# Kernel optimization log

Measured on AMD Instinct MI355X. Metric: run time of the kernel, lower is better.

Reference implementation:

```python
import jax, jax.numpy as jnp
import numpy as np

BS, NADJ, N, D_EMB, VOCAB = 2, 2, 2048, 64, 10000
H, F1 = 8, 64
NFEAT = 3 * D_EMB  # 192 = emb0(64) + emb1(64) + local(64)


def setup_inputs() -> dict:
    key = jax.random.key(0)
    ks = jax.random.split(key, 14)
    adj = jax.random.randint(ks[0], (BS, NADJ, N, N), 0, 2).astype(jnp.float32)
    adj = jnp.maximum(adj, jnp.eye(N, dtype=jnp.float32))  # self-loops: no empty softmax rows
    vertices = jax.random.randint(ks[1], (BS, N), 0, VOCAB)
    local_emb = jax.random.normal(ks[2], (BS, N, D_EMB), dtype=jnp.float32)
    xav = lambda fin, fout: (2.0 / (fin + fout)) ** 0.5
    emb0 = jax.random.normal(ks[3], (VOCAB, D_EMB), dtype=jnp.float32) * 0.02
    emb1 = jax.random.normal(ks[4], (VOCAB, D_EMB), dtype=jnp.float32) * 0.02
    w_l0 = jax.random.normal(ks[5], (NADJ, H, NFEAT, F1), dtype=jnp.float32) * xav(NFEAT, F1)
    a_src_l0 = jax.random.normal(ks[6], (NADJ, H, F1, 1), dtype=jnp.float32) * xav(F1, 1)
    a_dst_l0 = jax.random.normal(ks[7], (NADJ, H, F1, 1), dtype=jnp.float32) * xav(F1, 1)
    w_l1 = jax.random.normal(ks[8], (NADJ, H, H * F1, F1), dtype=jnp.float32) * xav(H * F1, F1)
    a_src_l1 = jax.random.normal(ks[9], (NADJ, H, F1, 1), dtype=jnp.float32) * xav(F1, 1)
    a_dst_l1 = jax.random.normal(ks[10], (NADJ, H, F1, 1), dtype=jnp.float32) * xav(F1, 1)
    aw1 = jax.random.normal(ks[11], (NFEAT, F1), dtype=jnp.float32) * xav(NFEAT, F1)
    aw2 = jax.random.normal(ks[12], (F1, F1), dtype=jnp.float32) * xav(F1, F1)
    am = jax.random.normal(ks[13], (F1, 1), dtype=jnp.float32) * xav(F1, 1)
    return dict(hedge_graphs=adj, vertices=vertices, local_emb=local_emb,
                emb0=emb0, emb1=emb1,
                w_l0=w_l0, a_src_l0=a_src_l0, a_dst_l0=a_dst_l0,
                w_l1=w_l1, a_src_l1=a_src_l1, a_dst_l1=a_dst_l1,
                aw1=aw1, aw2=aw2, am=am)


def _gat(h, adj, w, a_s, a_d):
    # h: (bs,N,f_in), w: (H,f_in,f_out), a_s/a_d: (H,f_out,1), adj: (bs,N,N)
    hp = jnp.einsum('bnf,hfo->bhno', h, w)             # (bs,H,N,f_out)
    t = jnp.tanh(hp)
    s = jnp.einsum('bhno,ho->bhn', t, a_s[..., 0])     # additive src score
    d = jnp.einsum('bhno,ho->bhn', t, a_d[..., 0])     # additive dst score
    attn = jax.nn.leaky_relu(s[:, :, :, None] + d[:, :, None, :], negative_slope=0.2)
    attn = jnp.where(adj[:, None, :, :] > 0, attn, -jnp.inf)
    attn = jax.nn.softmax(attn, axis=-1)               # masked softmax over neighbors
    return jnp.einsum('bhnm,bhmo->bhno', attn, hp)


def reference(hedge_graphs, vertices, local_emb, emb0, emb1,
              w_l0, a_src_l0, a_dst_l0, w_l1, a_src_l1, a_dst_l1,
              aw1, aw2, am):
    bs, n = vertices.shape
    feat = jnp.concatenate([emb0[vertices], emb1[vertices], local_emb], axis=2)  # (bs,N,192)
    h_embs = []
    for r in range(hedge_graphs.shape[1]):  # loop over relation types (small fixed)
        adj = hedge_graphs[:, r]
        h = _gat(feat, adj, w_l0[r], a_src_l0[r], a_dst_l0[r])          # (bs,H,N,F1)
        h = jnp.transpose(h, (0, 2, 1, 3)).reshape(bs, n, -1)           # concat heads
        h = jax.nn.elu(h)
        h = _gat(h, adj, w_l1[r], a_src_l1[r], a_dst_l1[r]).mean(axis=1)  # (bs,N,F1)
        h_embs.append(h)
    seq = jnp.stack(h_embs, axis=2)  # (bs,N,R,F1)
    # additive type-fusion attention
    q = jnp.tanh((feat @ aw1)[:, :, None, :] + seq @ aw2)  # (bs,N,R,F1)
    score = (q @ am)[..., 0]                               # (bs,N,R)
    beta = jax.nn.softmax(score, axis=-1)
    fused = jnp.einsum('bnr,bnrd->bnd', beta, seq)         # (bs,N,F1)
    return jax.nn.log_softmax(fused, axis=-1)
```

## Files before the change

### kernel.cpp

```cpp
#include <hip/hip_runtime.h>
#include <hip/hip_bf16.h>

#define BSZ 2
#define NADJ 2
#define NN 2048
#define DE 64
#define HH 8
#define F1 64
#define NF 192
#define K1 512
#define LOG2E 1.4426950408889634f

typedef short s16x8 __attribute__((ext_vector_type(8)));
typedef unsigned short u16x8 __attribute__((ext_vector_type(8)));
typedef float f32x4 __attribute__((ext_vector_type(4)));

#define GLOAD_LDS16(gp, lp)                                                    \
  __builtin_amdgcn_global_load_lds(                                            \
      (const __attribute__((address_space(1))) unsigned int*)(const void*)(gp),\
      (__attribute__((address_space(3))) unsigned int*)(void*)(lp), 16, 0, 0)

__device__ __forceinline__ unsigned short f2b(float x) {
  union { float f; unsigned int u; } v; v.f = x;
  unsigned int r = v.u + 0x7fffu + ((v.u >> 16) & 1u);
  return (unsigned short)(r >> 16);
}
__device__ __forceinline__ float b2f(unsigned short u) {
  union { unsigned int u; float f; } v; v.u = ((unsigned int)u) << 16;
  return v.f;
}

__device__ __forceinline__ const s16x8* tile_read_ptr(const unsigned short* lds,
                                                      int row, int kbyte) {
  return (const s16x8*)((const char*)lds + row * 128 + (kbyte ^ ((row & 7) << 4)));
}

__global__ __launch_bounds__(256) void k_build_feat(
    const int* __restrict__ vert, const float* __restrict__ lemb,
    const float* __restrict__ emb0, const float* __restrict__ emb1,
    unsigned short* __restrict__ featB) {
  int idx = blockIdx.x * 256 + threadIdx.x;
  int f = idx % NF;
  int bn = idx / NF;
  int v = vert[bn];
  float val;
  if (f < 64)       val = emb0[v * 64 + f];
  else if (f < 128) val = emb1[v * 64 + (f - 64)];
  else              val = lemb[bn * 64 + (f - 128)];
  featB[idx] = f2b(val);
}

__global__ __launch_bounds__(256) void k_bits(
    const float* __restrict__ hg, unsigned long long* __restrict__ bits) {
  size_t idx = (size_t)blockIdx.x * 256 + threadIdx.x;
  float a = hg[idx];
  unsigned long long m = __ballot(a > 0.f);
  if ((threadIdx.x & 63) == 0) bits[idx >> 6] = m;
}

__global__ __launch_bounds__(256) void k_tcast(
    const float* __restrict__ src, unsigned short* __restrict__ dst, int R) {
  __shared__ unsigned short tr[64][72];
  int k0 = blockIdx.x * 64;
  int plane = blockIdx.y;
  const float* s = src + (size_t)plane * R * 64;
  unsigned short* d = dst + (size_t)plane * 64 * R;
  int t = threadIdx.x;
#pragma unroll
  for (int q = 0; q < 4; ++q) {
    int e = q * 256 + t;
    int kr = e >> 4, oc = (e & 15) * 4;
    float4 v = *(const float4*)&s[(size_t)(k0 + kr) * 64 + oc];
    tr[oc + 0][kr] = f2b(v.x);
    tr[oc + 1][kr] = f2b(v.y);
    tr[oc + 2][kr] = f2b(v.z);
    tr[oc + 3][kr] = f2b(v.w);
  }
  __syncthreads();
#pragma unroll
  for (int q = 0; q < 2; ++q) {
    int e = q * 256 + t;
    int o = e >> 3, j8 = (e & 7) * 8;
    *(u16x8*)&d[(size_t)o * R + k0 + j8] = *(const u16x8*)&tr[o][j8];
  }
}

template <int K>
__global__ __launch_bounds__(256) void k_gemm_fused(
    const unsigned short* __restrict__ A, const unsigned short* __restrict__ Bw,
    const float* __restrict__ a_src, const float* __restrict__ a_dst,
    unsigned short* __restrict__ hpT, float2* __restrict__ sT,
    unsigned int* __restrict__ dT) {
  __shared__ unsigned short a_lds[2][64 * 64];
  __shared__ unsigned short b_lds[2][64 * 64];
  int tile = blockIdx.x, rh = blockIdx.y, b = blockIdx.z;
  int h = rh & 7, P = b * NADJ + (rh >> 3);
  int t = threadIdx.x, lane = t & 63, wv = t >> 6;
  const unsigned short* Ab = A + ((size_t)b * NN + tile * 64) * K;
  const unsigned short* Bb = Bw + (size_t)rh * 64 * K;
  const int NT = K / 64;
  int i0 = t, i1 = 256 + t;
  int o0 = i0 >> 3, o1 = i1 >> 3;
  size_t s0 = (size_t)o0 * K + (size_t)(((i0 & 7) ^ (o0 & 7)) * 8);
  size_t s1 = (size_t)o1 * K + (size_t)(((i1 & 7) ^ (o1 & 7)) * 8);
  int db0 = (wv * 64) * 8, db1 = (256 + wv * 64) * 8;

  GLOAD_LDS16(Ab + s0, a_lds[0] + db0);
  GLOAD_LDS16(Ab + s1, a_lds[0] + db1);
  GLOAD_LDS16(Bb + s0, b_lds[0] + db0);
  GLOAD_LDS16(Bb + s1, b_lds[0] + db1);
  __syncthreads();
  f32x4 acc[4] = {};
  int rowA = wv * 16 + (lane & 15);
  int rowB0 = lane & 15;
  int kb2 = (lane >> 4) * 16;
  for (int it = 0; it < NT; ++it) {
    int buf = it & 1;
    if (it + 1 < NT) {
      const unsigned short* As = Ab + (it + 1) * 64;
      const unsigned short* Bs = Bb + (it + 1) * 64;
      GLOAD_LDS16(As + s0, a_lds[buf ^ 1] + db0);
      GLOAD_LDS16(As + s1, a_lds[buf ^ 1] + db1);
      GLOAD_LDS16(Bs + s0, b_lds[buf ^ 1] + db0);
      GLOAD_LDS16(Bs + s1, b_lds[buf ^ 1] + db1);
    }
#pragma unroll
    for (int kk = 0; kk < 2; ++kk) {
      s16x8 av = *tile_read_ptr(a_lds[buf], rowA, kk * 64 + kb2);
#pragma unroll
      for (int nf = 0; nf < 4; ++nf) {
        s16x8 bv = *tile_read_ptr(b_lds[buf], nf * 16 + rowB0, kk * 64 + kb2);
        acc[nf] = __builtin_amdgcn_mfma_f32_16x16x32_bf16(av, bv, acc[nf], 0, 0, 0);
      }
    }
    __syncthreads();
  }
  float sp[4] = {}, dp[4] = {};
#pragma unroll
  for (int nf = 0; nf < 4; ++nf) {
    int c = nf * 16 + (lane & 15);
    float as = a_src[rh * 64 + c], ad = a_dst[rh * 64 + c];
#pragma unroll
    for (int reg = 0; reg < 4; ++reg) {
      float x = acc[nf][reg];
      x = fminf(fmaxf(x, -30.f), 30.f);
      float e2 = __builtin_amdgcn_exp2f(x * (2.f * LOG2E));
      float th = (e2 - 1.f) * __builtin_amdgcn_rcpf(e2 + 1.f);
      sp[reg] += th * as;
      dp[reg] += th * ad;
    }
  }
#pragma unroll
  for (int reg = 0; reg < 4; ++reg) {
#pragma unroll
    for (int off = 8; off; off >>= 1) {
      sp[reg] += __shfl_xor(sp[reg], off);
      dp[reg] += __shfl_xor(dp[reg], off);
    }
  }
  if ((lane & 15) == 0) {
#pragma unroll
    for (int reg = 0; reg < 4; ++reg) {
      int m = tile * 64 + wv * 16 + (lane >> 4) * 4 + reg;
      float sv = sp[reg] * LOG2E, dv = dp[reg] * LOG2E;
      sT[(size_t)P * NN * HH + (size_t)m * HH + h] =
          make_float2(__builtin_amdgcn_exp2f(sv), __builtin_amdgcn_exp2f(0.2f * sv));
      float Ed = __builtin_amdgcn_exp2f(dv), Ed2 = __builtin_amdgcn_exp2f(0.2f * dv);
      dT[((size_t)P * HH + h) * NN + m] =
          ((unsigned int)f2b(Ed) << 16) | (unsigned int)f2b(Ed2);
    }
  }
  unsigned short* tr = a_lds[0];
#pragma unroll
  for (int nf = 0; nf < 4; ++nf) {
    int c = nf * 16 + (lane & 15);
#pragma unroll
    for (int reg = 0; reg < 4; ++reg) {
      int m = wv * 16 + (lane >> 4) * 4 + reg;
      tr[c * 76 + m] = f2b(acc[nf][reg]);
    }
  }
  __syncthreads();
  unsigned short* dst = hpT + ((size_t)P * HH + h) * 64 * NN + tile * 64;
#pragma unroll
  for (int q = 0; q < 2; ++q) {
    int e = q * 256 + t;
    int o = e >> 3, j8 = (e & 7) * 8;
    u16x8 v;
#pragma unroll
    for (int z = 0; z < 8; ++z) v[z] = tr[o * 76 + j8 + z];
    *(u16x8*)&dst[(size_t)o * NN + j8] = v;
  }
}

__global__ __launch_bounds__(512) void k_gemm_fused_ks(
    const unsigned short* __restrict__ A, const unsigned short* __restrict__ Bw,
    const float* __restrict__ a_src, const float* __restrict__ a_dst,
    unsigned short* __restrict__ hpT, float2* __restrict__ sT,
    unsigned int* __restrict__ dT) {
  __shared__ unsigned short a_lds[2][2][64 * 64];
  __shared__ unsigned short b_lds[2][2][64 * 64];
  const int K = K1;
  int tile = blockIdx.x, h = blockIdx.y, P = blockIdx.z;
  int rh = (P & 1) * HH + h;
  int t = threadIdx.x, lane = t & 63;
  int wid = t >> 6, g = wid >> 2, wv = wid & 3;
  int tg = t & 255;
  const unsigned short* Ab = A + ((size_t)P * NN + tile * 64) * K + g * 256;
  const unsigned short* Bb = Bw + (size_t)rh * 64 * K + g * 256;
  const int NT = 4;
  int i0 = tg, i1 = 256 + tg;
  int o0 = i0 >> 3, o1 = i1 >> 3;
  size_t s0 = (size_t)o0 * K + (size_t)(((i0 & 7) ^ (o0 & 7)) * 8);
  size_t s1 = (size_t)o1 * K + (size_t)(((i1 & 7) ^ (o1 & 7)) * 8);
  int db0 = (wv * 64) * 8, db1 = (256 + wv * 64) * 8;

  GLOAD_LDS16(Ab + s0, a_lds[g][0] + db0);
  GLOAD_LDS16(Ab + s1, a_lds[g][0] + db1);
  GLOAD_LDS16(Bb + s0, b_lds[g][0] + db0);
  GLOAD_LDS16(Bb + s1, b_lds[g][0] + db1);
  __syncthreads();
  f32x4 acc[4] = {};
  int rowA = wv * 16 + (lane & 15);
  int rowB0 = lane & 15;
  int kb2 = (lane >> 4) * 16;
  for (int it = 0; it < NT; ++it) {
    int buf = it & 1;
    if (it + 1 < NT) {
      const unsigned short* As = Ab + (it + 1) * 64;
      const unsigned short* Bs = Bb + (it + 1) * 64;
      GLOAD_LDS16(As + s0, a_lds[g][buf ^ 1] + db0);
      GLOAD_LDS16(As + s1, a_lds[g][buf ^ 1] + db1);
      GLOAD_LDS16(Bs + s0, b_lds[g][buf ^ 1] + db0);
      GLOAD_LDS16(Bs + s1, b_lds[g][buf ^ 1] + db1);
    }
#pragma unroll
    for (int kk = 0; kk < 2; ++kk) {
      s16x8 av = *tile_read_ptr(a_lds[g][buf], rowA, kk * 64 + kb2);
#pragma unroll
      for (int nf = 0; nf < 4; ++nf) {
        s16x8 bv = *tile_read_ptr(b_lds[g][buf], nf * 16 + rowB0, kk * 64 + kb2);
        acc[nf] = __builtin_amdgcn_mfma_f32_16x16x32_bf16(av, bv, acc[nf], 0, 0, 0);
      }
    }
    __syncthreads();
  }
  float* comb = (float*)&a_lds[0][0][0];
  if (g == 1) {
    float* dst = comb + (wv * 64 + lane) * 17;
#pragma unroll
    for (int nf = 0; nf < 4; ++nf)
#pragma unroll
      for (int reg = 0; reg < 4; ++reg) dst[nf * 4 + reg] = acc[nf][reg];
  }
  __syncthreads();
  if (g == 0) {
    const float* srcp = comb + (wv * 64 + lane) * 17;
#pragma unroll
    for (int nf = 0; nf < 4; ++nf)
#pragma unroll
      for (int reg = 0; reg < 4; ++reg) acc[nf][reg] += srcp[nf * 4 + reg];
    float sp[4] = {}, dp[4] = {};
#pragma unroll
    for (int nf = 0; nf < 4; ++nf) {
      int c = nf * 16 + (lane & 15);
      float as = a_src[rh * 64 + c], ad = a_dst[rh * 64 + c];
#pragma unroll
      for (int reg = 0; reg < 4; ++reg) {
        float x = acc[nf][reg];
        x = fminf(fmaxf(x, -30.f), 30.f);
        float e2 = __builtin_amdgcn_exp2f(x * (2.f * LOG2E));
        float th = (e2 - 1.f) * __builtin_amdgcn_rcpf(e2 + 1.f);
        sp[reg] += th * as;
        dp[reg] += th * ad;
      }
    }
#pragma unroll
    for (int reg = 0; reg < 4; ++reg) {
#pragma unroll
      for (int off = 8; off; off >>= 1) {
        sp[reg] += __shfl_xor(sp[reg], off);
        dp[reg] += __shfl_xor(dp[reg], off);
      }
    }
    if ((lane & 15) == 0) {
#pragma unroll
      for (int reg = 0; reg < 4; ++reg) {
        int m = tile * 64 + wv * 16 + (lane >> 4) * 4 + reg;
        float sv = sp[reg] * LOG2E, dv = dp[reg] * LOG2E;
        sT[(size_t)P * NN * HH + (size_t)m * HH + h] =
            make_float2(__builtin_amdgcn_exp2f(sv), __builtin_amdgcn_exp2f(0.2f * sv));
        float Ed = __builtin_amdgcn_exp2f(dv), Ed2 = __builtin_amdgcn_exp2f(0.2f * dv);
        dT[((size_t)P * HH + h) * NN + m] =
            ((unsigned int)f2b(Ed) << 16) | (unsigned int)f2b(Ed2);
      }
    }
    unsigned short* tr = (unsigned short*)&b_lds[0][0][0];
#pragma unroll
    for (int nf = 0; nf < 4; ++nf) {
      int c = nf * 16 + (lane & 15);
#pragma unroll
      for (int reg = 0; reg < 4; ++reg) {
        int m = wv * 16 + (lane >> 4) * 4 + reg;
        tr[c * 76 + m] = f2b(acc[nf][reg]);
      }
    }
  }
  __syncthreads();
  if (g == 0) {
    const unsigned short* tr = (const unsigned short*)&b_lds[0][0][0];
    unsigned short* dst = hpT + ((size_t)P * HH + h) * 64 * NN + tile * 64;
#pragma unroll
    for (int q = 0; q < 2; ++q) {
      int e = q * 256 + tg;
      int o = e >> 3, j8 = (e & 7) * 8;
      u16x8 v;
#pragma unroll
      for (int z = 0; z < 8; ++z) v[z] = tr[o * 76 + j8 + z];
      *(u16x8*)&dst[(size_t)o * NN + j8] = v;
    }
  }
}

template <int MODE>
__global__ __launch_bounds__(512) void k_pv(
    const unsigned long long* __restrict__ bits,
    const unsigned short* __restrict__ hpT,
    const float2* __restrict__ sT, const unsigned int* __restrict__ dT,
    unsigned short* __restrict__ outB) {
  __shared__ unsigned short hp_lds[2][2][64 * 64];
  __shared__ unsigned int d_all[2][1024];
  int i0 = blockIdx.x * 64, h = blockIdx.y, P = blockIdx.z;
  int t = threadIdx.x, lane = t & 63;
  int wid = t >> 6, g = wid >> 2, wv = wid & 3;
  int tg = t & 255;
  int rowi = wv * 16 + (lane & 15);
  int kb = (lane >> 4) * 8;
  float2 se = sT[(size_t)P * NN * HH + (size_t)(i0 + rowi) * HH + h];
  float Es = se.x, Es2 = se.y;
  const unsigned long long* brow =
      bits + ((size_t)P * NN + i0 + rowi) * 32 + g * 16;
  const unsigned short* hpTb = hpT + ((size_t)P * HH + h) * 64 * NN + g * 1024;
  const unsigned int* dTb = dT + ((size_t)P * HH + h) * NN + g * 1024;
  f32x4 acc[4] = {};
  f32x4 accl = {};
  const short ONE = (short)0x3F80;
  const s16x8 ones = {ONE, ONE, ONE, ONE, ONE, ONE, ONE, ONE};

  int idx0 = (wv * 2 + 0) * 64 + lane;
  int idx1 = (wv * 2 + 1) * 64 + lane;
  int o0 = idx0 >> 3, o1 = idx1 >> 3;
  size_t soff0 = (size_t)o0 * NN + (size_t)(((idx0 & 7) ^ (o0 & 7)) * 8);
  size_t soff1 = (size_t)o1 * NN + (size_t)(((idx1 & 7) ^ (o1 & 7)) * 8);
  unsigned short* c0  = hp_lds[g][0] + (wv * 2 + 0) * 512;
  unsigned short* c1  = hp_lds[g][0] + (wv * 2 + 1) * 512;
  unsigned short* c0b = hp_lds[g][1] + (wv * 2 + 0) * 512;
  unsigned short* c1b = hp_lds[g][1] + (wv * 2 + 1) * 512;

  GLOAD_LDS16(hpTb + soff0, c0);
  GLOAD_LDS16(hpTb + soff1, c1);
  {
    uint4 dv4 = *(const uint4*)&dTb[tg * 4];
    *(uint4*)&d_all[g][tg * 4] = dv4;
  }
  unsigned long long bw = brow[0];
  __syncthreads();

  const int NT = 16;
  for (int it = 0; it < NT; ++it) {
    int buf = it & 1;
    if (it + 1 < NT) {
      const unsigned short* src = hpTb + (it + 1) * 64;
      if (buf) { GLOAD_LDS16(src + soff0, c0);  GLOAD_LDS16(src + soff1, c1); }
      else     { GLOAD_LDS16(src + soff0, c0b); GLOAD_LDS16(src + soff1, c1b); }
    }
    unsigned long long bwn = (it + 1 < NT) ? brow[it + 1] : 0ull;
    unsigned int bsel[2];
    bsel[0] = (unsigned int)(bw >> kb);
    bsel[1] = (unsigned int)(bw >> (32 + kb));
    union { unsigned int u[4]; s16x8 v; } af[2];
#pragma unroll
    for (int kk = 0; kk < 2; ++kk) {
      const unsigned int* dpk = &d_all[g][it * 64 + kk * 32 + kb];
      uint4 p0 = *(const uint4*)(dpk);
      uint4 p1 = *(const uint4*)(dpk + 4);
      unsigned int pk8[8] = {p0.x, p0.y, p0.z, p0.w, p1.x, p1.y, p1.z, p1.w};
      float w8[8];
#pragma unroll
      for (int c = 0; c < 8; ++c) {
        int msk = ((int)(bsel[kk] << (31 - c))) >> 31;
        unsigned int pm = pk8[c] & (unsigned int)msk;
        float Ed  = __uint_as_float(pm & 0xffff0000u);
        float Ed2 = __uint_as_float(pm << 16);
        w8[c] = fmaxf(Es * Ed, Es2 * Ed2);
      }
#pragma unroll
      for (int p = 0; p < 4; ++p) {
        unsigned int pk;
        asm volatile("v_cvt_pk_bf16_f32 %0, %1, %2"
                     : "=v"(pk) : "v"(w8[2 * p]), "v"(w8[2 * p + 1]));
        af[kk].u[p] = pk;
      }
    }
#pragma unroll
    for (int kk = 0; kk < 2; ++kk) {
#pragma unroll
      for (int nf = 0; nf < 4; ++nf) {
        s16x8 bv = *tile_read_ptr(hp_lds[g][buf], nf * 16 + (lane & 15),
                                  kk * 64 + (lane >> 4) * 16);
        acc[nf] = __builtin_amdgcn_mfma_f32_16x16x32_bf16(af[kk].v, bv, acc[nf], 0, 0, 0);
      }
      accl = __builtin_amdgcn_mfma_f32_16x16x32_bf16(af[kk].v, ones, accl, 0, 0, 0);
    }
    bw = bwn;
    __syncthreads();
  }
  float* comb = (float*)&hp_lds[0][0][0];
  if (g == 1) {
    float* dst = comb + (wv * 64 + lane) * 21;
#pragma unroll
    for (int nf = 0; nf < 4; ++nf)
#pragma unroll
      for (int reg = 0; reg < 4; ++reg) dst[nf * 4 + reg] = acc[nf][reg];
#pragma unroll
    for (int reg = 0; reg < 4; ++reg) dst[16 + reg] = accl[reg];
  }
  __syncthreads();
  if (g == 0) {
    const float* srcp = comb + (wv * 64 + lane) * 21;
#pragma unroll
    for (int nf = 0; nf < 4; ++nf)
#pragma unroll
      for (int reg = 0; reg < 4; ++reg) acc[nf][reg] += srcp[nf * 4 + reg];
#pragma unroll
    for (int reg = 0; reg < 4; ++reg) accl[reg] += srcp[16 + reg];
    int col = lane & 15, r0g = (lane >> 4) * 4;
#pragma unroll
    for (int reg = 0; reg < 4; ++reg) {
      int m = wv * 16 + r0g + reg;
      float linv = 1.0f / accl[reg];
      if (MODE == 0) {
        size_t ob = (((size_t)P * HH + h) * NN + i0 + m) * 64 + col;
#pragma unroll
        for (int nf = 0; nf < 4; ++nf)
          outB[ob + nf * 16] = f2b(acc[nf][reg] * linv);
      } else {
        size_t ob = ((size_t)P * NN + i0 + m) * K1 + h * 64 + col;
#pragma unroll
        for (int nf = 0; nf < 4; ++nf) {
          float v = acc[nf][reg] * linv;
          v = v > 0.f ? v : (__builtin_amdgcn_exp2f(v * LOG2E) - 1.f);
          outB[ob + nf * 16] = f2b(v);
        }
      }
    }
  }
}

__global__ __launch_bounds__(256) void k_mean(
    const unsigned short* __restrict__ in, float* __restrict__ seq) {
  int idx = blockIdx.x * 256 + threadIdx.x;
  int o8 = (idx & 7) * 8;
  int n = (idx >> 3) & (NN - 1);
  int P = idx >> 14;
  int b = P >> 1, r = P & 1;
  float acc[8] = {};
#pragma unroll
  for (int h = 0; h < HH; ++h) {
    u16x8 v = *(const u16x8*)&in[(((size_t)P * HH + h) * NN + n) * 64 + o8];
#pragma unroll
    for (int z = 0; z < 8; ++z) acc[z] += b2f((unsigned short)v[z]);
  }
  float* dst = &seq[(((size_t)b * NN + n) * NADJ + r) * 64 + o8];
#pragma unroll
  for (int z = 0; z < 8; ++z) dst[z] = acc[z] * 0.125f;
}

__global__ __launch_bounds__(256) void k_fuse(
    const unsigned short* __restrict__ featB, const float* __restrict__ aw1,
    const float* __restrict__ seq, const float* __restrict__ aw2,
    const float* __restrict__ am, float* __restrict__ outp) {
  __shared__ float w2[64][65];
  __shared__ float a1[NF][64];
  __shared__ float amv[64];
  __shared__ unsigned short feat_l[4][NF];
  __shared__ float seq_lds[4][NADJ][64];
  int t = threadIdx.x;
#pragma unroll
  for (int q = 0; q < 16; ++q) {
    int e = t + 256 * q;
    w2[e >> 6][e & 63] = aw2[e];
  }
  float* a1f = &a1[0][0];
#pragma unroll
  for (int q = 0; q < 12; ++q) {
    int e4 = (t + 256 * q) * 4;
    *(float4*)&a1f[e4] = *(const float4*)&aw1[e4];
  }
  if (t < 64) amv[t] = am[t];
  int wid = t >> 6, lane = t & 63;
  int bn = blockIdx.x * 4 + wid;
  if (lane < 24)
    *(u16x8*)&feat_l[wid][lane * 8] = *(const u16x8*)&featB[(size_t)bn * NF + lane * 8];
  float s0 = seq[((size_t)bn * NADJ + 0) * 64 + lane];
  float s1 = seq[((size_t)bn * NADJ + 1) * 64 + lane];
  seq_lds[wid][0][lane] = s0;
  seq_lds[wid][1][lane] = s1;
  __syncthreads();
  float f = 0.f;
#pragma unroll 4
  for (int kc = 0; kc < NF / 8; ++kc) {
    u16x8 fv = *(const u16x8*)&feat_l[wid][kc * 8];
#pragma unroll
    for (int z = 0; z < 8; ++z)
      f += b2f((unsigned short)fv[z]) * a1[kc * 8 + z][lane];
  }
  float q0 = f, q1 = f;
  for (int k = 0; k < 64; ++k) {
    float wv = w2[k][lane];
    q0 += seq_lds[wid][0][k] * wv;
    q1 += seq_lds[wid][1][k] * wv;
  }
  q0 = tanhf(q0); q1 = tanhf(q1);
  float sc0 = q0 * amv[lane], sc1 = q1 * amv[lane];
  for (int off = 32; off; off >>= 1) {
    sc0 += __shfl_xor(sc0, off);
    sc1 += __shfl_xor(sc1, off);
  }
  float mx = fmaxf(sc0, sc1);
  float e0 = __expf(sc0 - mx), e1 = __expf(sc1 - mx);
  float inv = 1.f / (e0 + e1);
  float fu = (e0 * inv) * s0 + (e1 * inv) * s1;
  float m = fu;
  for (int off = 32; off; off >>= 1) m = fmaxf(m, __shfl_xor(m, off));
  float ex = __expf(fu - m);
  float ssum = ex;
  for (int off = 32; off; off >>= 1) ssum += __shfl_xor(ssum, off);
  outp[(size_t)bn * 64 + lane] = fu - m - __logf(ssum);
}

extern "C" void kernel_launch(void* const* d_in, const int* in_sizes, int n_in,
                              void* d_out, int out_size, void* d_ws, size_t ws_size,
                              hipStream_t stream) {
  (void)in_sizes; (void)n_in; (void)out_size; (void)ws_size;
  const float* hg   = (const float*)d_in[0];
  const int*   vert = (const int*)d_in[1];
  const float* lemb = (const float*)d_in[2];
  const float* emb0 = (const float*)d_in[3];
  const float* emb1 = (const float*)d_in[4];
  const float* w_l0 = (const float*)d_in[5];
  const float* as0  = (const float*)d_in[6];
  const float* ad0  = (const float*)d_in[7];
  const float* w_l1 = (const float*)d_in[8];
  const float* as1  = (const float*)d_in[9];
  const float* ad1  = (const float*)d_in[10];
  const float* aw1  = (const float*)d_in[11];
  const float* aw2  = (const float*)d_in[12];
  const float* am   = (const float*)d_in[13];
  float* out = (float*)d_out;

  const int NP = BSZ * NADJ;
  char* p = (char*)d_ws;
  unsigned short* hpT   = (unsigned short*)p;  p += (size_t)NP*HH*NN*64*2;
  unsigned short* aoutB = (unsigned short*)p;  p += (size_t)NP*HH*NN*64*2;
  unsigned short* hmidB = (unsigned short*)p;  p += (size_t)NP*NN*K1*2;
  unsigned short* featB = (unsigned short*)p;  p += (size_t)BSZ*NN*NF*2;
  unsigned short* wT0   = (unsigned short*)p;  p += (size_t)NADJ*HH*64*NF*2;
  unsigned short* wT1   = (unsigned short*)p;  p += (size_t)NADJ*HH*64*K1*2;
  float2* sT            = (float2*)p;          p += (size_t)NP*NN*HH*8;
  unsigned int* dT      = (unsigned int*)p;    p += (size_t)NP*HH*NN*4;
  unsigned long long* bits = (unsigned long long*)p; p += (size_t)NP*NN*(NN/64)*8;
  float* seq            = (float*)p;           p += (size_t)BSZ*NN*NADJ*64*4;

  k_build_feat<<<(BSZ*NN*NF)/256, 256, 0, stream>>>(vert, lemb, emb0, emb1, featB);
  k_bits<<<(size_t)NP*NN*NN/256, 256, 0, stream>>>(hg, bits);
  k_tcast<<<dim3(NF/64, NADJ*HH), 256, 0, stream>>>(w_l0, wT0, NF);
  k_tcast<<<dim3(K1/64, NADJ*HH), 256, 0, stream>>>(w_l1, wT1, K1);

  k_gemm_fused<NF><<<dim3(NN/64, NADJ*HH, BSZ), 256, 0, stream>>>(
      featB, wT0, as0, ad0, hpT, sT, dT);
  k_pv<1><<<dim3(NN/64, HH, NP), 512, 0, stream>>>(bits, hpT, sT, dT, hmidB);
  k_gemm_fused_ks<<<dim3(NN/64, HH, NP), 512, 0, stream>>>(
      hmidB, wT1, as1, ad1, hpT, sT, dT);
  k_pv<0><<<dim3(NN/64, HH, NP), 512, 0, stream>>>(bits, hpT, sT, dT, aoutB);
  k_mean<<<(NP*NN*8)/256, 256, 0, stream>>>(aoutB, seq);

  k_fuse<<<BSZ*NN/4, 256, 0, stream>>>(featB, aw1, seq, aw2, am, out);
}
```

Before: 157.4 us.

## Halve k_pv waves so each wave computes two 16-row tiles sharing B-fragment reads

The attention-times-values kernel k_pv now launches 256 threads instead of 512. Each wave handles two 16-row groups, so every LDS read of the hp tile feeds two MFMAs, which halves shared-memory reads per MFMA. Each thread now issues four global-to-LDS loads per stage instead of two, and MFMA issue is wrapped in s_setprio. The cost is more registers per thread from doubled accumulators and fewer waves to hide latency.

```diff
diff --git a/kernel.cpp b/kernel.cpp
--- a/kernel.cpp
+++ b/kernel.cpp
@@ -323,7 +323,7 @@
 }
 
 template <int MODE>
-__global__ __launch_bounds__(512) void k_pv(
+__global__ __launch_bounds__(256) void k_pv(
     const unsigned long long* __restrict__ bits,
     const unsigned short* __restrict__ hpT,
     const float2* __restrict__ sT, const unsigned int* __restrict__ dT,
@@ -332,38 +332,55 @@
   __shared__ unsigned int d_all[2][1024];
   int i0 = blockIdx.x * 64, h = blockIdx.y, P = blockIdx.z;
   int t = threadIdx.x, lane = t & 63;
-  int wid = t >> 6, g = wid >> 2, wv = wid & 3;
-  int tg = t & 255;
-  int rowi = wv * 16 + (lane & 15);
+  int wid = t >> 6;
+  int rw = wid & 1;
+  int g  = wid >> 1;
+  int tg = t & 127;
   int kb = (lane >> 4) * 8;
-  float2 se = sT[(size_t)P * NN * HH + (size_t)(i0 + rowi) * HH + h];
-  float Es = se.x, Es2 = se.y;
-  const unsigned long long* brow =
-      bits + ((size_t)P * NN + i0 + rowi) * 32 + g * 16;
+  int row0 = rw * 32 + (lane & 15);
+  float2 se0 = sT[(size_t)P * NN * HH + (size_t)(i0 + row0) * HH + h];
+  float2 se1 = sT[(size_t)P * NN * HH + (size_t)(i0 + row0 + 16) * HH + h];
+  const unsigned long long* brow0 =
+      bits + ((size_t)P * NN + i0 + row0) * 32 + g * 16;
+  const unsigned long long* brow1 = brow0 + 16 * 32;
   const unsigned short* hpTb = hpT + ((size_t)P * HH + h) * 64 * NN + g * 1024;
   const unsigned int* dTb = dT + ((size_t)P * HH + h) * NN + g * 1024;
-  f32x4 acc[4] = {};
-  f32x4 accl = {};
+  f32x4 acc[2][4] = {};
+  f32x4 accl0 = {}, accl1 = {};
   const short ONE = (short)0x3F80;
   const s16x8 ones = {ONE, ONE, ONE, ONE, ONE, ONE, ONE, ONE};
 
-  int idx0 = (wv * 2 + 0) * 64 + lane;
-  int idx1 = (wv * 2 + 1) * 64 + lane;
-  int o0 = idx0 >> 3, o1 = idx1 >> 3;
-  size_t soff0 = (size_t)o0 * NN + (size_t)(((idx0 & 7) ^ (o0 & 7)) * 8);
-  size_t soff1 = (size_t)o1 * NN + (size_t)(((idx1 & 7) ^ (o1 & 7)) * 8);
-  unsigned short* c0  = hp_lds[g][0] + (wv * 2 + 0) * 512;
-  unsigned short* c1  = hp_lds[g][0] + (wv * 2 + 1) * 512;
-  unsigned short* c0b = hp_lds[g][1] + (wv * 2 + 0) * 512;
-  unsigned short* c1b = hp_lds[g][1] + (wv * 2 + 1) * 512;
-
-  GLOAD_LDS16(hpTb + soff0, c0);
-  GLOAD_LDS16(hpTb + soff1, c1);
+  size_t soff0, soff1, soff2, soff3;
   {
-    uint4 dv4 = *(const uint4*)&dTb[tg * 4];
-    *(uint4*)&d_all[g][tg * 4] = dv4;
-  }
-  unsigned long long bw = brow[0];
+    int idx, o;
+    idx = 0 * 128 + tg; o = idx >> 3;
+    soff0 = (size_t)o * NN + (size_t)((((idx & 7) ^ (o & 7))) * 8);
+    idx = 1 * 128 + tg; o = idx >> 3;
+    soff1 = (size_t)o * NN + (size_t)((((idx & 7) ^ (o & 7))) * 8);
+    idx = 2 * 128 + tg; o = idx >> 3;
+    soff2 = (size_t)o * NN + (size_t)((((idx & 7) ^ (o & 7))) * 8);
+    idx = 3 * 128 + tg; o = idx >> 3;
+    soff3 = (size_t)o * NN + (size_t)((((idx & 7) ^ (o & 7))) * 8);
+  }
+  int db0 = (0 * 128 + rw * 64) * 8;
+  int db1 = (1 * 128 + rw * 64) * 8;
+  int db2 = (2 * 128 + rw * 64) * 8;
+  int db3 = (3 * 128 + rw * 64) * 8;
+
+  {
+    unsigned short* db = hp_lds[g][0];
+    GLOAD_LDS16(hpTb + soff0, db + db0);
+    GLOAD_LDS16(hpTb + soff1, db + db1);
+    GLOAD_LDS16(hpTb + soff2, db + db2);
+    GLOAD_LDS16(hpTb + soff3, db + db3);
+  }
+  {
+    uint4 dv0 = *(const uint4*)&dTb[tg * 8];
+    uint4 dv1 = *(const uint4*)&dTb[tg * 8 + 4];
+    *(uint4*)&d_all[g][tg * 8] = dv0;
+    *(uint4*)&d_all[g][tg * 8 + 4] = dv1;
+  }
+  unsigned long long bw0 = brow0[0], bw1 = brow1[0];
   __syncthreads();
 
   const int NT = 16;
@@ -371,86 +388,115 @@
     int buf = it & 1;
     if (it + 1 < NT) {
       const unsigned short* src = hpTb + (it + 1) * 64;
-      if (buf) { GLOAD_LDS16(src + soff0, c0);  GLOAD_LDS16(src + soff1, c1); }
-      else     { GLOAD_LDS16(src + soff0, c0b); GLOAD_LDS16(src + soff1, c1b); }
-    }
-    unsigned long long bwn = (it + 1 < NT) ? brow[it + 1] : 0ull;
-    unsigned int bsel[2];
-    bsel[0] = (unsigned int)(bw >> kb);
-    bsel[1] = (unsigned int)(bw >> (32 + kb));
-    union { unsigned int u[4]; s16x8 v; } af[2];
+      unsigned short* db = hp_lds[g][buf ^ 1];
+      GLOAD_LDS16(src + soff0, db + db0);
+      GLOAD_LDS16(src + soff1, db + db1);
+      GLOAD_LDS16(src + soff2, db + db2);
+      GLOAD_LDS16(src + soff3, db + db3);
+    }
+    unsigned long long bwn0 = 0, bwn1 = 0;
+    if (it + 1 < NT) { bwn0 = brow0[it + 1]; bwn1 = brow1[it + 1]; }
+    union { unsigned int u[4]; s16x8 v; } af[2][2];
 #pragma unroll
     for (int kk = 0; kk < 2; ++kk) {
       const unsigned int* dpk = &d_all[g][it * 64 + kk * 32 + kb];
       uint4 p0 = *(const uint4*)(dpk);
       uint4 p1 = *(const uint4*)(dpk + 4);
       unsigned int pk8[8] = {p0.x, p0.y, p0.z, p0.w, p1.x, p1.y, p1.z, p1.w};
-      float w8[8];
-#pragma unroll
-      for (int c = 0; c < 8; ++c) {
-        int msk = ((int)(bsel[kk] << (31 - c))) >> 31;
-        unsigned int pm = pk8[c] & (unsigned int)msk;
-        float Ed  = __uint_as_float(pm & 0xffff0000u);
-        float Ed2 = __uint_as_float(pm << 16);
-        w8[c] = fmaxf(Es * Ed, Es2 * Ed2);
-      }
-#pragma unroll
-      for (int p = 0; p < 4; ++p) {
-        unsigned int pk;
-        asm volatile("v_cvt_pk_bf16_f32 %0, %1, %2"
-                     : "=v"(pk) : "v"(w8[2 * p]), "v"(w8[2 * p + 1]));
-        af[kk].u[p] = pk;
-      }
-    }
+      unsigned int bs0 = (unsigned int)(bw0 >> (kk * 32 + kb));
+      unsigned int bs1 = (unsigned int)(bw1 >> (kk * 32 + kb));
+#pragma unroll
+      for (int rg = 0; rg < 2; ++rg) {
+        float Es  = rg ? se1.x : se0.x;
+        float Es2 = rg ? se1.y : se0.y;
+        unsigned int bs = rg ? bs1 : bs0;
+        float w8[8];
+#pragma unroll
+        for (int c = 0; c < 8; ++c) {
+          int msk = ((int)(bs << (31 - c))) >> 31;
+          unsigned int pm = pk8[c] & (unsigned int)msk;
+          float Ed  = __uint_as_float(pm & 0xffff0000u);
+          float Ed2 = __uint_as_float(pm << 16);
+          w8[c] = fmaxf(Es * Ed, Es2 * Ed2);
+        }
+#pragma unroll
+        for (int p = 0; p < 4; ++p) {
+          unsigned int pk;
+          asm volatile("v_cvt_pk_bf16_f32 %0, %1, %2"
+                       : "=v"(pk) : "v"(w8[2 * p]), "v"(w8[2 * p + 1]));
+          af[rg][kk].u[p] = pk;
+        }
+      }
+    }
+    __builtin_amdgcn_s_setprio(1);
 #pragma unroll
     for (int kk = 0; kk < 2; ++kk) {
 #pragma unroll
       for (int nf = 0; nf < 4; ++nf) {
         s16x8 bv = *tile_read_ptr(hp_lds[g][buf], nf * 16 + (lane & 15),
                                   kk * 64 + (lane >> 4) * 16);
-        acc[nf] = __builtin_amdgcn_mfma_f32_16x16x32_bf16(af[kk].v, bv, acc[nf], 0, 0, 0);
-      }
-      accl = __builtin_amdgcn_mfma_f32_16x16x32_bf16(af[kk].v, ones, accl, 0, 0, 0);
-    }
-    bw = bwn;
+        acc[0][nf] = __builtin_amdgcn_mfma_f32_16x16x32_bf16(af[0][kk].v, bv, acc[0][nf], 0, 0, 0);
+        acc[1][nf] = __builtin_amdgcn_mfma_f32_16x16x32_bf16(af[1][kk].v, bv, acc[1][nf], 0, 0, 0);
+      }
+      accl0 = __builtin_amdgcn_mfma_f32_16x16x32_bf16(af[0][kk].v, ones, accl0, 0, 0, 0);
+      accl1 = __builtin_amdgcn_mfma_f32_16x16x32_bf16(af[1][kk].v, ones, accl1, 0, 0, 0);
+    }
+    __builtin_amdgcn_s_setprio(0);
+    bw0 = bwn0; bw1 = bwn1;
     __syncthreads();
   }
   float* comb = (float*)&hp_lds[0][0][0];
   if (g == 1) {
-    float* dst = comb + (wv * 64 + lane) * 21;
-#pragma unroll
-    for (int nf = 0; nf < 4; ++nf)
-#pragma unroll
-      for (int reg = 0; reg < 4; ++reg) dst[nf * 4 + reg] = acc[nf][reg];
-#pragma unroll
-    for (int reg = 0; reg < 4; ++reg) dst[16 + reg] = accl[reg];
+    float* dst = comb + tg * 41;
+#pragma unroll
+    for (int rg = 0; rg < 2; ++rg)
+#pragma unroll
+      for (int nf = 0; nf < 4; ++nf)
+#pragma unroll
+        for (int reg = 0; reg < 4; ++reg)
+          dst[rg * 16 + nf * 4 + reg] = acc[rg][nf][reg];
+#pragma unroll
+    for (int reg = 0; reg < 4; ++reg) {
+      dst[32 + reg] = accl0[reg];
+      dst[36 + reg] = accl1[reg];
+    }
   }
   __syncthreads();
   if (g == 0) {
-    const float* srcp = comb + (wv * 64 + lane) * 21;
-#pragma unroll
-    for (int nf = 0; nf < 4; ++nf)
-#pragma unroll
-      for (int reg = 0; reg < 4; ++reg) acc[nf][reg] += srcp[nf * 4 + reg];
-#pragma unroll
-    for (int reg = 0; reg < 4; ++reg) accl[reg] += srcp[16 + reg];
+    const float* srcp = comb + tg * 41;
+#pragma unroll
+    for (int rg = 0; rg < 2; ++rg)
+#pragma unroll
+      for (int nf = 0; nf < 4; ++nf)
+#pragma unroll
+        for (int reg = 0; reg < 4; ++reg)
+          acc[rg][nf][reg] += srcp[rg * 16 + nf * 4 + reg];
+#pragma unroll
+    for (int reg = 0; reg < 4; ++reg) {
+      accl0[reg] += srcp[32 + reg];
+      accl1[reg] += srcp[36 + reg];
+    }
     int col = lane & 15, r0g = (lane >> 4) * 4;
 #pragma unroll
-    for (int reg = 0; reg < 4; ++reg) {
-      int m = wv * 16 + r0g + reg;
-      float linv = 1.0f / accl[reg];
-      if (MODE == 0) {
-        size_t ob = (((size_t)P * HH + h) * NN + i0 + m) * 64 + col;
-#pragma unroll
-        for (int nf = 0; nf < 4; ++nf)
-          outB[ob + nf * 16] = f2b(acc[nf][reg] * linv);
-      } else {
-        size_t ob = ((size_t)P * NN + i0 + m) * K1 + h * 64 + col;
-#pragma unroll
-        for (int nf = 0; nf < 4; ++nf) {
-          float v = acc[nf][reg] * linv;
-          v = v > 0.f ? v : (__builtin_amdgcn_exp2f(v * LOG2E) - 1.f);
-          outB[ob + nf * 16] = f2b(v);
+    for (int rg = 0; rg < 2; ++rg) {
+#pragma unroll
+      for (int reg = 0; reg < 4; ++reg) {
+        int m = rw * 32 + rg * 16 + r0g + reg;
+        float lv = rg ? accl1[reg] : accl0[reg];
+        float linv = 1.0f / lv;
+        if (MODE == 0) {
+          size_t ob = (((size_t)P * HH + h) * NN + i0 + m) * 64 + col;
+#pragma unroll
+          for (int nf = 0; nf < 4; ++nf)
+            outB[ob + nf * 16] = f2b(acc[rg][nf][reg] * linv);
+        } else {
+          size_t ob = ((size_t)P * NN + i0 + m) * K1 + h * 64 + col;
+#pragma unroll
+          for (int nf = 0; nf < 4; ++nf) {
+            float v = acc[rg][nf][reg] * linv;
+            v = v > 0.f ? v : (__builtin_amdgcn_exp2f(v * LOG2E) - 1.f);
+            outB[ob + nf * 16] = f2b(v);
+          }
         }
       }
     }
@@ -579,10 +625,10 @@
 
   k_gemm_fused<NF><<<dim3(NN/64, NADJ*HH, BSZ), 256, 0, stream>>>(
       featB, wT0, as0, ad0, hpT, sT, dT);
-  k_pv<1><<<dim3(NN/64, HH, NP), 512, 0, stream>>>(bits, hpT, sT, dT, hmidB);
+  k_pv<1><<<dim3(NN/64, HH, NP), 256, 0, stream>>>(bits, hpT, sT, dT, hmidB);
   k_gemm_fused_ks<<<dim3(NN/64, HH, NP), 512, 0, stream>>>(
       hmidB, wT1, as1, ad1, hpT, sT, dT);
-  k_pv<0><<<dim3(NN/64, HH, NP), 512, 0, stream>>>(bits, hpT, sT, dT, aoutB);
+  k_pv<0><<<dim3(NN/64, HH, NP), 256, 0, stream>>>(bits, hpT, sT, dT, aoutB);
   k_mean<<<(NP*NN*8)/256, 256, 0, stream>>>(aoutB, seq);
 
   k_fuse<<<BSZ*NN/4, 256, 0, stream>>>(featB, aw1, seq, aw2, am, out);
```

After: 160.3 us. About the same (+1.8%).
